# Performance work log

Hardware: AMD Instinct MI355X
Metric: run time of the kernel (lower is better)

The kernel has to match this reference:

```python
import jax, jax.numpy as jnp
import numpy as np

B, L, D, MELS, VOCAB, MAXDUR = 16, 256, 512, 80, 256, 12
T_MAX = L * MAXDUR  # 3072, upper bound on expanded mel length


def setup_inputs() -> dict:
    key = jax.random.key(0)
    ks = jax.random.split(key, 10)
    s = 1.0 / np.sqrt(D)
    return {
        "src": jax.random.randint(ks[0], (B, L), 0, VOCAB),
        "input_dur_inframe": jax.random.randint(ks[1], (B, L), 0, MAXDUR),
        "T": T_MAX,
        "emb_table": jax.random.normal(ks[2], (VOCAB, D), jnp.float32),
        "pos_table": jax.random.normal(ks[3], (L, D), jnp.float32),
        "W_enc": jax.random.normal(ks[4], (D, D), jnp.float32) * s,
        "b_enc": jnp.zeros((D,), jnp.float32),
        "W_dur": jax.random.normal(ks[5], (D, 1), jnp.float32) * s,
        "b_dur": jnp.zeros((1,), jnp.float32),
        "W_dec": jax.random.normal(ks[6], (D, D), jnp.float32) * s,
        "b_dec": jnp.zeros((D,), jnp.float32),
        "W_gen": jax.random.normal(ks[7], (D, MELS), jnp.float32) * s,
        "b_gen": jnp.zeros((MELS,), jnp.float32),
    }


def length_regulate(enc, dur, T):
    """Vectorized equivalent of the nested per-(batch, token) scatter loop.
    Frame f of batch j copies enc[j, k] where k is the token whose duration
    span covers f; frames past the total duration stay zero."""
    csum = jnp.cumsum(dur, axis=-1)                      # [B, L]
    frames = jnp.arange(T)                               # [T]
    # token index per frame: count of tokens with csum <= f
    tok = jax.vmap(lambda c: jnp.searchsorted(c, frames, side="right"))(csum)  # [B, T]
    valid = (tok < dur.shape[1])[..., None]               # [B, T, 1]
    tok = jnp.minimum(tok, dur.shape[1] - 1)
    out = jnp.take_along_axis(enc, tok[..., None], axis=1)  # [B, T, D]
    return out * valid


def reference(src, input_dur_inframe, T, emb_table, pos_table,
              W_enc, b_enc, W_dur, b_dur, W_dec, b_dec, W_gen, b_gen):
    # encode: embedding + positional embedding -> encoder
    x = emb_table[src] + pos_table[None, : src.shape[1], :]        # [B, L, D]
    enc = jax.nn.relu(x @ W_enc + b_enc)                            # [B, L, D]
    # duration predictor on encoder output
    dur_pred = (enc @ W_dur + b_dur)[..., 0]                        # [B, L]
    # length regulator (the custom-kernel hot spot)
    outp = length_regulate(enc, input_dur_inframe, T)               # [B, T, D]
    # decoder + generator, then permute to [B, n_mels, T]
    dec = jax.nn.relu(outp @ W_dec + b_dec)                         # [B, T, D]
    mel = jnp.transpose(dec @ W_gen + b_gen, (0, 2, 1))             # [B, MELS, T]
    return mel, dur_pred
```

## Files before the change

kernel.cpp:

```cpp
#include <hip/hip_runtime.h>

#define D_ 512
#define L_ 256
#define B_ 16
#define T_ 3072
#define MELS_ 80
#define R_ 4096
#define RZ_ 4097
#define CS_ 4104

typedef __bf16 bf16x8 __attribute__((ext_vector_type(8)));
typedef float f32x4 __attribute__((ext_vector_type(4)));

__device__ __forceinline__ unsigned f2bf(float f) {
  union { float f; unsigned u; } x; x.f = f;
  return (x.u + 0x7FFFu + ((x.u >> 16) & 1u)) >> 16;
}
__device__ __forceinline__ float bf2f(unsigned h) {
  union { unsigned u; float f; } x; x.u = h << 16;
  return x.f;
}

__device__ __forceinline__ void transw_dev(const float* __restrict__ src,
                                           unsigned short* __restrict__ dst,
                                           int N, int local, float* sh) {
  int kt = local & 7, nt = local >> 3;
  int k0 = kt * 64, n0 = nt * 64;
  int tid = threadIdx.x;
  int c = tid & 63, r4 = tid >> 6;
  for (int it = 0; it < 16; ++it) {
    int r = it * 4 + r4;
    int n = n0 + c;
    sh[r * 65 + c] = (n < N) ? src[(k0 + r) * N + n] : 0.f;
  }
  __syncthreads();
  for (int it = 0; it < 16; ++it) {
    int r = it * 4 + r4;
    int n = n0 + r;
    if (n < N) dst[n * D_ + k0 + c] = (unsigned short)f2bf(sh[c * 65 + r]);
  }
}

__device__ __forceinline__ void tok_dev(const int* __restrict__ dur,
                                        int* __restrict__ TOK, int b, int* cs) {
  int tid = threadIdx.x;
  cs[tid] = dur[b * L_ + tid];
  for (int off = 1; off < L_; off <<= 1) {
    __syncthreads();
    int v = (tid >= off) ? cs[tid - off] : 0;
    __syncthreads();
    cs[tid] += v;
  }
  __syncthreads();
  for (int t = tid; t < T_; t += 256) {
    int lo = 0, hi = L_;
    while (lo < hi) { int mid = (lo + hi) >> 1; if (cs[mid] <= t) lo = mid + 1; else hi = mid; }
    TOK[b * T_ + t] = (lo < L_) ? (b * L_ + lo) : R_;
  }
}

__global__ void prep_all(const int* __restrict__ src, const int* __restrict__ dur,
                         const float* __restrict__ emb, const float* __restrict__ pos,
                         const float* __restrict__ Wenc, const float* __restrict__ Wdec,
                         const float* __restrict__ Wgen,
                         unsigned short* __restrict__ X, unsigned short* __restrict__ ENC,
                         unsigned short* __restrict__ WET, unsigned short* __restrict__ WDT,
                         unsigned short* __restrict__ WGT, int* __restrict__ TOK) {
  __shared__ float sh[64 * 65];
  int bid = blockIdx.x, tid = threadIdx.x;
  if (bid < 1024) {
    int row = bid * 4 + (tid >> 6);
    int lane = tid & 63;
    int s = src[row];
    int l = row & (L_ - 1);
    int d = lane * 8;
    const float4* ep = (const float4*)(emb + (size_t)s * D_ + d);
    const float4* pp = (const float4*)(pos + (size_t)l * D_ + d);
    float4 a0 = ep[0], a1 = ep[1];
    float4 b0 = pp[0], b1 = pp[1];
    uint4 o;
    o.x = f2bf(a0.x + b0.x) | (f2bf(a0.y + b0.y) << 16);
    o.y = f2bf(a0.z + b0.z) | (f2bf(a0.w + b0.w) << 16);
    o.z = f2bf(a1.x + b1.x) | (f2bf(a1.y + b1.y) << 16);
    o.w = f2bf(a1.z + b1.z) | (f2bf(a1.w + b1.w) << 16);
    *(uint4*)(X + (size_t)row * D_ + d) = o;
  } else if (bid == 1024) {
    if (tid < 64) {
      uint4 z = {0u, 0u, 0u, 0u};
      *(uint4*)(ENC + (size_t)R_ * D_ + tid * 8) = z;
    }
  } else if (bid < 1089) {
    transw_dev(Wenc, WET, 512, bid - 1025, sh);
  } else if (bid < 1153) {
    transw_dev(Wdec, WDT, 512, bid - 1089, sh);
  } else if (bid < 1169) {
    transw_dev(Wgen, WGT, MELS_, bid - 1153, sh);
  } else {
    tok_dev(dur, TOK, bid - 1169, (int*)sh);
  }
}

__global__ __launch_bounds__(256, 4) void gemm64(
    const unsigned short* __restrict__ A, const unsigned short* __restrict__ Bt,
    const float* __restrict__ bias, unsigned short* __restrict__ C,
    int mclamp, int mstore, int ngemm,
    const float* __restrict__ wdur, const float* __restrict__ bdur,
    float* __restrict__ durout) {
  __shared__ short lsA[64 * 64];
  __shared__ short lsB[64 * 64];
  int bid = blockIdx.x, tid = threadIdx.x;
  int lane = tid & 63, w = tid >> 6;

  if (bid >= ngemm) {
    int row = (bid - ngemm) * 4 + w;
    const uint4 e = *(const uint4*)(A + (size_t)row * D_ + lane * 8);
    float4 w0 = *(const float4*)(wdur + lane * 8);
    float4 w1 = *(const float4*)(wdur + lane * 8 + 4);
    float s = 0.f;
    s += bf2f(e.x & 0xffffu) * w0.x;  s += bf2f(e.x >> 16) * w0.y;
    s += bf2f(e.y & 0xffffu) * w0.z;  s += bf2f(e.y >> 16) * w0.w;
    s += bf2f(e.z & 0xffffu) * w1.x;  s += bf2f(e.z >> 16) * w1.y;
    s += bf2f(e.w & 0xffffu) * w1.z;  s += bf2f(e.w >> 16) * w1.w;
    for (int off = 32; off > 0; off >>= 1) s += __shfl_down(s, off, 64);
    if (lane == 0) durout[row] = s + bdur[0];
    return;
  }

  int wm = w >> 1, wn = w & 1;
  int col = lane & 15, quad = lane >> 4;
  int m0 = (bid >> 3) * 64, n0 = (bid & 7) * 64;
  f32x4 acc[2][2] = {};
  for (int ks = 0; ks < 8; ++ks) {
    int k0 = ks * 64;
    __syncthreads();
    for (int it = 0; it < 2; ++it) {
      int linear = it * 256 + tid;
      int row = linear >> 3, p = linear & 7;
      int seg = (p + row) & 7;
      const unsigned short* ga = A + (size_t)min(m0 + row, mclamp) * D_ + k0 + seg * 8;
      const unsigned short* gb = Bt + (size_t)(n0 + row) * D_ + k0 + seg * 8;
      short* la = lsA + (size_t)(it * 256 + (tid & ~63)) * 8;
      short* lb = lsB + (size_t)(it * 256 + (tid & ~63)) * 8;
      __builtin_amdgcn_global_load_lds((const __attribute__((address_space(1))) void*)ga,
                                       (__attribute__((address_space(3))) void*)la, 16, 0, 0);
      __builtin_amdgcn_global_load_lds((const __attribute__((address_space(1))) void*)gb,
                                       (__attribute__((address_space(3))) void*)lb, 16, 0, 0);
    }
    __syncthreads();
    for (int kk = 0; kk < 2; ++kk) {
      int s = kk * 4 + quad;
      bf16x8 af[2], bfr[2];
      for (int mt = 0; mt < 2; ++mt) {
        int r = wm * 32 + mt * 16 + col;
        int p = (s - r) & 7;
        af[mt] = *(const bf16x8*)(lsA + ((size_t)r * 8 + p) * 8);
      }
      for (int nt = 0; nt < 2; ++nt) {
        int r = wn * 32 + nt * 16 + col;
        int p = (s - r) & 7;
        bfr[nt] = *(const bf16x8*)(lsB + ((size_t)r * 8 + p) * 8);
      }
      for (int mt = 0; mt < 2; ++mt)
        for (int nt = 0; nt < 2; ++nt)
          acc[mt][nt] = __builtin_amdgcn_mfma_f32_16x16x32_bf16(af[mt], bfr[nt], acc[mt][nt], 0, 0, 0);
    }
  }
  for (int nt = 0; nt < 2; ++nt) {
    int n = n0 + wn * 32 + nt * 16 + col;
    float bn = bias[n];
    for (int mt = 0; mt < 2; ++mt) {
      int mb = m0 + wm * 32 + mt * 16 + quad * 4;
      for (int i = 0; i < 4; ++i) {
        int m = mb + i;
        if (m < mstore) {
          float v = acc[mt][nt][i] + bn;
          v = v > 0.f ? v : 0.f;
          C[(size_t)m * D_ + n] = (unsigned short)f2bf(v);
        }
      }
    }
  }
}

__global__ void genk(const unsigned short* __restrict__ dec, const unsigned short* __restrict__ wgT,
                     const float* __restrict__ bgen, float* __restrict__ melT) {
  __shared__ float sh[4 * 80 * 16];
  int tid = threadIdx.x;
  int lane = tid & 63, w = tid >> 6;
  int col = lane & 15, quad = lane >> 4;
  int n0 = blockIdx.x * 16;
  int n = n0 + col;
  int nc = min(n, R_);
  f32x4 acc[5] = {};
  const unsigned short* dp = dec + (size_t)nc * D_ + quad * 8;
  for (int ks = 0; ks < 4; ++ks) {
    int k0 = (w * 4 + ks) * 32;
    bf16x8 bfr = *(const bf16x8*)(dp + k0);
    for (int mt = 0; mt < 5; ++mt) {
      bf16x8 afr = *(const bf16x8*)(wgT + (size_t)(mt * 16 + col) * D_ + k0 + quad * 8);
      acc[mt] = __builtin_amdgcn_mfma_f32_16x16x32_bf16(afr, bfr, acc[mt], 0, 0, 0);
    }
  }
  for (int mt = 0; mt < 5; ++mt)
    for (int i = 0; i < 4; ++i) {
      int m = mt * 16 + quad * 4 + i;
      sh[w * 1280 + m * 16 + col] = acc[mt][i];
    }
  __syncthreads();
  for (int j = 0; j < 5; ++j) {
    int idx = j * 256 + tid;
    float v = sh[idx] + sh[1280 + idx] + sh[2560 + idx] + sh[3840 + idx];
    int m = idx >> 4;
    int nn = n0 + (idx & 15);
    if (nn <= R_) melT[(size_t)m * CS_ + nn] = v + bgen[m];
  }
}

__global__ void outk(const int* __restrict__ TOK, const float* __restrict__ melT,
                     float* __restrict__ out) {
  int b = blockIdx.y;
  int tl = blockIdx.x * 128 + (threadIdx.x & 31) * 4;
  int m0 = threadIdx.x >> 5;
  int4 tg = *(const int4*)(TOK + b * T_ + tl);
  float* ob = out + (size_t)b * MELS_ * T_ + tl;
  for (int it = 0; it < 10; ++it) {
    int m = m0 + it * 8;
    const float* mr = melT + (size_t)m * CS_;
    float4 v = make_float4(mr[tg.x], mr[tg.y], mr[tg.z], mr[tg.w]);
    *(float4*)(ob + (size_t)m * T_) = v;
  }
}

extern "C" void kernel_launch(void* const* d_in, const int* in_sizes, int n_in,
                              void* d_out, int out_size, void* d_ws, size_t ws_size,
                              hipStream_t stream) {
  const int* src = (const int*)d_in[0];
  const int* dur = (const int*)d_in[1];
  const float* emb = (const float*)d_in[3];
  const float* pos = (const float*)d_in[4];
  const float* Wenc = (const float*)d_in[5];
  const float* benc = (const float*)d_in[6];
  const float* Wdur = (const float*)d_in[7];
  const float* bdur = (const float*)d_in[8];
  const float* Wdec = (const float*)d_in[9];
  const float* bdec = (const float*)d_in[10];
  const float* Wgen = (const float*)d_in[11];
  const float* bgen = (const float*)d_in[12];

  char* ws = (char*)d_ws;
  unsigned short* X   = (unsigned short*)(ws + 0);
  unsigned short* ENC = (unsigned short*)(ws + 4194304);
  unsigned short* DEC = (unsigned short*)(ws + 8389632);
  unsigned short* WET = (unsigned short*)(ws + 12584960);
  unsigned short* WDT = (unsigned short*)(ws + 13109248);
  unsigned short* WGT = (unsigned short*)(ws + 13633536);
  int* TOK            = (int*)(ws + 13715456);
  float* MELT         = (float*)(ws + 13912064);

  float* out = (float*)d_out;
  float* durout = out + (size_t)B_ * MELS_ * T_;

  prep_all<<<1185, 256, 0, stream>>>(src, dur, emb, pos, Wenc, Wdec, Wgen,
                                     X, ENC, WET, WDT, WGT, TOK);
  gemm64<<<512, 256, 0, stream>>>(X, WET, benc, ENC, R_ - 1, R_, 512,
                                  nullptr, nullptr, nullptr);
  gemm64<<<1544, 256, 0, stream>>>(ENC, WDT, bdec, DEC, R_, RZ_, 520,
                                   Wdur, bdur, durout);
  genk<<<257, 256, 0, stream>>>(DEC, WGT, bgen, MELT);
  outk<<<dim3(24, 16), 256, 0, stream>>>(TOK, MELT, out);
}
```

Baseline: 127.8 us.

## Overlap weight transposes and token search with encoder GEMM, widen K tile

Moves the Wdec/Wgen transposes and the duration prefix-sum/token search out of the prep kernel and into extra blocks of the encoder GEMM launch, so they run alongside the GEMM tiles. The GEMM tile now stages 128-wide K slices in LDS (32KB) instead of 64, halving the barrier-separated K iterations. The embedding prep processes two rows per wave and the duration dot-product blocks handle 16 rows each, reducing block counts. The larger LDS footprint may reduce occupancy.

```diff
diff --git a/kernel.cpp b/kernel.cpp
--- a/kernel.cpp
+++ b/kernel.cpp
@@ -6,7 +6,6 @@
 #define T_ 3072
 #define MELS_ 80
 #define R_ 4096
-#define RZ_ 4097
 #define CS_ 4104
 
 typedef __bf16 bf16x8 __attribute__((ext_vector_type(8)));
@@ -59,84 +58,22 @@
   }
 }
 
-__global__ void prep_all(const int* __restrict__ src, const int* __restrict__ dur,
-                         const float* __restrict__ emb, const float* __restrict__ pos,
-                         const float* __restrict__ Wenc, const float* __restrict__ Wdec,
-                         const float* __restrict__ Wgen,
-                         unsigned short* __restrict__ X, unsigned short* __restrict__ ENC,
-                         unsigned short* __restrict__ WET, unsigned short* __restrict__ WDT,
-                         unsigned short* __restrict__ WGT, int* __restrict__ TOK) {
-  __shared__ float sh[64 * 65];
-  int bid = blockIdx.x, tid = threadIdx.x;
-  if (bid < 1024) {
-    int row = bid * 4 + (tid >> 6);
-    int lane = tid & 63;
-    int s = src[row];
-    int l = row & (L_ - 1);
-    int d = lane * 8;
-    const float4* ep = (const float4*)(emb + (size_t)s * D_ + d);
-    const float4* pp = (const float4*)(pos + (size_t)l * D_ + d);
-    float4 a0 = ep[0], a1 = ep[1];
-    float4 b0 = pp[0], b1 = pp[1];
-    uint4 o;
-    o.x = f2bf(a0.x + b0.x) | (f2bf(a0.y + b0.y) << 16);
-    o.y = f2bf(a0.z + b0.z) | (f2bf(a0.w + b0.w) << 16);
-    o.z = f2bf(a1.x + b1.x) | (f2bf(a1.y + b1.y) << 16);
-    o.w = f2bf(a1.z + b1.z) | (f2bf(a1.w + b1.w) << 16);
-    *(uint4*)(X + (size_t)row * D_ + d) = o;
-  } else if (bid == 1024) {
-    if (tid < 64) {
-      uint4 z = {0u, 0u, 0u, 0u};
-      *(uint4*)(ENC + (size_t)R_ * D_ + tid * 8) = z;
-    }
-  } else if (bid < 1089) {
-    transw_dev(Wenc, WET, 512, bid - 1025, sh);
-  } else if (bid < 1153) {
-    transw_dev(Wdec, WDT, 512, bid - 1089, sh);
-  } else if (bid < 1169) {
-    transw_dev(Wgen, WGT, MELS_, bid - 1153, sh);
-  } else {
-    tok_dev(dur, TOK, bid - 1169, (int*)sh);
-  }
-}
-
-__global__ __launch_bounds__(256, 4) void gemm64(
+__device__ __forceinline__ void gemm_tile(
     const unsigned short* __restrict__ A, const unsigned short* __restrict__ Bt,
     const float* __restrict__ bias, unsigned short* __restrict__ C,
-    int mclamp, int mstore, int ngemm,
-    const float* __restrict__ wdur, const float* __restrict__ bdur,
-    float* __restrict__ durout) {
-  __shared__ short lsA[64 * 64];
-  __shared__ short lsB[64 * 64];
-  int bid = blockIdx.x, tid = threadIdx.x;
+    int m0, int n0, int mclamp, int mstore, short* lsA, short* lsB) {
+  int tid = threadIdx.x;
   int lane = tid & 63, w = tid >> 6;
-
-  if (bid >= ngemm) {
-    int row = (bid - ngemm) * 4 + w;
-    const uint4 e = *(const uint4*)(A + (size_t)row * D_ + lane * 8);
-    float4 w0 = *(const float4*)(wdur + lane * 8);
-    float4 w1 = *(const float4*)(wdur + lane * 8 + 4);
-    float s = 0.f;
-    s += bf2f(e.x & 0xffffu) * w0.x;  s += bf2f(e.x >> 16) * w0.y;
-    s += bf2f(e.y & 0xffffu) * w0.z;  s += bf2f(e.y >> 16) * w0.w;
-    s += bf2f(e.z & 0xffffu) * w1.x;  s += bf2f(e.z >> 16) * w1.y;
-    s += bf2f(e.w & 0xffffu) * w1.z;  s += bf2f(e.w >> 16) * w1.w;
-    for (int off = 32; off > 0; off >>= 1) s += __shfl_down(s, off, 64);
-    if (lane == 0) durout[row] = s + bdur[0];
-    return;
-  }
-
   int wm = w >> 1, wn = w & 1;
   int col = lane & 15, quad = lane >> 4;
-  int m0 = (bid >> 3) * 64, n0 = (bid & 7) * 64;
   f32x4 acc[2][2] = {};
-  for (int ks = 0; ks < 8; ++ks) {
-    int k0 = ks * 64;
-    __syncthreads();
-    for (int it = 0; it < 2; ++it) {
+  for (int ks = 0; ks < 4; ++ks) {
+    int k0 = ks * 128;
+    __syncthreads();
+    for (int it = 0; it < 4; ++it) {
       int linear = it * 256 + tid;
-      int row = linear >> 3, p = linear & 7;
-      int seg = (p + row) & 7;
+      int row = linear >> 4, p = linear & 15;
+      int seg = (p + row) & 15;
       const unsigned short* ga = A + (size_t)min(m0 + row, mclamp) * D_ + k0 + seg * 8;
       const unsigned short* gb = Bt + (size_t)(n0 + row) * D_ + k0 + seg * 8;
       short* la = lsA + (size_t)(it * 256 + (tid & ~63)) * 8;
@@ -147,18 +84,16 @@
                                        (__attribute__((address_space(3))) void*)lb, 16, 0, 0);
     }
     __syncthreads();
-    for (int kk = 0; kk < 2; ++kk) {
+    for (int kk = 0; kk < 4; ++kk) {
       int s = kk * 4 + quad;
       bf16x8 af[2], bfr[2];
       for (int mt = 0; mt < 2; ++mt) {
         int r = wm * 32 + mt * 16 + col;
-        int p = (s - r) & 7;
-        af[mt] = *(const bf16x8*)(lsA + ((size_t)r * 8 + p) * 8);
+        af[mt] = *(const bf16x8*)(lsA + (size_t)r * 128 + ((s - r) & 15) * 8);
       }
       for (int nt = 0; nt < 2; ++nt) {
         int r = wn * 32 + nt * 16 + col;
-        int p = (s - r) & 7;
-        bfr[nt] = *(const bf16x8*)(lsB + ((size_t)r * 8 + p) * 8);
+        bfr[nt] = *(const bf16x8*)(lsB + (size_t)r * 128 + ((s - r) & 15) * 8);
       }
       for (int mt = 0; mt < 2; ++mt)
         for (int nt = 0; nt < 2; ++nt)
@@ -182,6 +117,91 @@
   }
 }
 
+__global__ void prep1(const int* __restrict__ src, const float* __restrict__ emb,
+                      const float* __restrict__ pos, const float* __restrict__ Wenc,
+                      unsigned short* __restrict__ X, unsigned short* __restrict__ WET,
+                      unsigned short* __restrict__ ENC) {
+  __shared__ float sh[64 * 65];
+  int bid = blockIdx.x, tid = threadIdx.x;
+  if (bid < 512) {
+    int lane = tid & 63, w = tid >> 6;
+    for (int u = 0; u < 2; ++u) {
+      int row = bid * 8 + u * 4 + w;
+      int s = src[row];
+      int l = row & (L_ - 1);
+      int d = lane * 8;
+      const float4* ep = (const float4*)(emb + (size_t)s * D_ + d);
+      const float4* pp = (const float4*)(pos + (size_t)l * D_ + d);
+      float4 a0 = ep[0], a1 = ep[1];
+      float4 b0 = pp[0], b1 = pp[1];
+      uint4 o;
+      o.x = f2bf(a0.x + b0.x) | (f2bf(a0.y + b0.y) << 16);
+      o.y = f2bf(a0.z + b0.z) | (f2bf(a0.w + b0.w) << 16);
+      o.z = f2bf(a1.x + b1.x) | (f2bf(a1.y + b1.y) << 16);
+      o.w = f2bf(a1.z + b1.z) | (f2bf(a1.w + b1.w) << 16);
+      *(uint4*)(X + (size_t)row * D_ + d) = o;
+    }
+  } else if (bid < 576) {
+    transw_dev(Wenc, WET, 512, bid - 512, sh);
+  } else {
+    if (tid < 64) {
+      uint4 z = {0u, 0u, 0u, 0u};
+      *(uint4*)(ENC + (size_t)R_ * D_ + (tid & 63) * 8) = z;
+    }
+  }
+}
+
+__global__ __launch_bounds__(256, 4) void gemm_enc(
+    const unsigned short* __restrict__ X, const unsigned short* __restrict__ WET,
+    const float* __restrict__ benc, unsigned short* __restrict__ ENC,
+    const float* __restrict__ Wdec, const float* __restrict__ Wgen,
+    const int* __restrict__ dur,
+    unsigned short* __restrict__ WDT, unsigned short* __restrict__ WGT,
+    int* __restrict__ TOK) {
+  __shared__ __align__(16) char smem[32768];
+  int bid = blockIdx.x;
+  if (bid < 512) {
+    gemm_tile(X, WET, benc, ENC, (bid >> 3) * 64, (bid & 7) * 64, R_ - 1, R_,
+              (short*)smem, (short*)(smem + 16384));
+  } else if (bid < 576) {
+    transw_dev(Wdec, WDT, 512, bid - 512, (float*)smem);
+  } else if (bid < 592) {
+    transw_dev(Wgen, WGT, MELS_, bid - 576, (float*)smem);
+  } else {
+    tok_dev(dur, TOK, bid - 592, (int*)smem);
+  }
+}
+
+__global__ __launch_bounds__(256, 4) void gemm_dec(
+    const unsigned short* __restrict__ ENC, const unsigned short* __restrict__ WDT,
+    const float* __restrict__ bdec, unsigned short* __restrict__ DEC,
+    const float* __restrict__ wdur, const float* __restrict__ bdur,
+    float* __restrict__ durout) {
+  __shared__ __align__(16) char smem[32768];
+  int bid = blockIdx.x, tid = threadIdx.x;
+  int lane = tid & 63, w = tid >> 6;
+  if (bid >= 520) {
+    int b2 = bid - 520;
+    float4 w0 = *(const float4*)(wdur + lane * 8);
+    float4 w1 = *(const float4*)(wdur + lane * 8 + 4);
+    float bv = bdur[0];
+    for (int rep = 0; rep < 4; ++rep) {
+      int row = b2 * 16 + w * 4 + rep;
+      const uint4 e = *(const uint4*)(ENC + (size_t)row * D_ + lane * 8);
+      float s = 0.f;
+      s += bf2f(e.x & 0xffffu) * w0.x;  s += bf2f(e.x >> 16) * w0.y;
+      s += bf2f(e.y & 0xffffu) * w0.z;  s += bf2f(e.y >> 16) * w0.w;
+      s += bf2f(e.z & 0xffffu) * w1.x;  s += bf2f(e.z >> 16) * w1.y;
+      s += bf2f(e.w & 0xffffu) * w1.z;  s += bf2f(e.w >> 16) * w1.w;
+      for (int off = 32; off > 0; off >>= 1) s += __shfl_down(s, off, 64);
+      if (lane == 0) durout[row] = s + bv;
+    }
+    return;
+  }
+  gemm_tile(ENC, WDT, bdec, DEC, (bid >> 3) * 64, (bid & 7) * 64, R_, R_ + 1,
+            (short*)smem, (short*)(smem + 16384));
+}
+
 __global__ void genk(const unsigned short* __restrict__ dec, const unsigned short* __restrict__ wgT,
                      const float* __restrict__ bgen, float* __restrict__ melT) {
   __shared__ float sh[4 * 80 * 16];
@@ -202,10 +222,8 @@
     }
   }
   for (int mt = 0; mt < 5; ++mt)
-    for (int i = 0; i < 4; ++i) {
-      int m = mt * 16 + quad * 4 + i;
-      sh[w * 1280 + m * 16 + col] = acc[mt][i];
-    }
+    for (int i = 0; i < 4; ++i)
+      sh[w * 1280 + (mt * 16 + quad * 4 + i) * 16 + col] = acc[mt][i];
   __syncthreads();
   for (int j = 0; j < 5; ++j) {
     int idx = j * 256 + tid;
@@ -260,12 +278,9 @@
   float* out = (float*)d_out;
   float* durout = out + (size_t)B_ * MELS_ * T_;
 
-  prep_all<<<1185, 256, 0, stream>>>(src, dur, emb, pos, Wenc, Wdec, Wgen,
-                                     X, ENC, WET, WDT, WGT, TOK);
-  gemm64<<<512, 256, 0, stream>>>(X, WET, benc, ENC, R_ - 1, R_, 512,
-                                  nullptr, nullptr, nullptr);
-  gemm64<<<1544, 256, 0, stream>>>(ENC, WDT, bdec, DEC, R_, RZ_, 520,
-                                   Wdur, bdur, durout);
+  prep1<<<577, 256, 0, stream>>>(src, emb, pos, Wenc, X, WET, ENC);
+  gemm_enc<<<608, 256, 0, stream>>>(X, WET, benc, ENC, Wdec, Wgen, dur, WDT, WGT, TOK);
+  gemm_dec<<<776, 256, 0, stream>>>(ENC, WDT, bdec, DEC, Wdur, bdur, durout);
   genk<<<257, 256, 0, stream>>>(DEC, WGT, bgen, MELT);
   outk<<<dim3(24, 16), 256, 0, stream>>>(TOK, MELT, out);
 }
```

Result: faster. 121.7 us (median of 2 runs) (-4.8%).
